# Kernel tuning notes

Measured on AMD Instinct MI355X. Metric: run time of the kernel, lower is better.

Reference implementation:

```python
import jax, jax.numpy as jnp
import numpy as np

N, E, D, H, L = 50000, 800000, 64, 128, 3  # nodes, edges, embed dim, mlp hidden (2*D), layers
HDIM, EDIM, G = 8, 8, 10
EPS_MSG = 1e-7
BN_EPS = 1e-5
LN_EPS = 1e-5


def setup_inputs() -> dict:
    key = jax.random.key(0)
    ks = jax.random.split(key, 12)
    s = lambda f: 1.0 / np.sqrt(f)
    return {
        "x": jax.random.normal(ks[0], (N, HDIM), jnp.float32),
        "edge_index": jax.random.randint(ks[1], (2, E), 0, N, dtype=jnp.int32),
        "edge_attr": jax.random.normal(ks[2], (E, EDIM), jnp.float32),
        "node_W": jax.random.normal(ks[3], (HDIM, D), jnp.float32) * s(HDIM),
        "node_b": jnp.zeros((D,), jnp.float32),
        "edge_W": jax.random.normal(ks[4], (EDIM, D), jnp.float32) * s(EDIM),
        "edge_b": jnp.zeros((D,), jnp.float32),
        "bn_gamma": jnp.ones((L, D), jnp.float32),
        "bn_beta": jnp.zeros((L, D), jnp.float32),
        "t": jnp.ones((L,), jnp.float32),
        "W1": jax.random.normal(ks[5], (L, D, H), jnp.float32) * s(D),
        "b1": jnp.zeros((L, H), jnp.float32),
        "ln_g": jnp.ones((L, H), jnp.float32),
        "ln_b": jnp.zeros((L, H), jnp.float32),
        "W2": jax.random.normal(ks[6], (L, H, D), jnp.float32) * s(H),
        "b2": jnp.zeros((L, D), jnp.float32),
        "num_graphs": G,
    }


def _layer(h, src, dst, e, g, b, t_i, W1i, b1i, lg, lb, W2i, b2i):
    # DeepGCNLayer 'res+': out = x + conv(relu(BN(x)))
    mu = h.mean(0)
    var = h.var(0)  # biased, as torch BN normalization
    hn = jax.nn.relu((h - mu) / jnp.sqrt(var + BN_EPS) * g + b)
    # GENConv message: relu(x_j + edge_attr) + eps
    msg = jax.nn.relu(hn[src] + e) + EPS_MSG  # [E, D]
    # softmax aggregation per destination node, per channel, with temperature t
    logits = msg * t_i
    m = jax.ops.segment_max(logits, dst, num_segments=N)
    m = jnp.where(jnp.isfinite(m), m, 0.0)
    a = jnp.exp(logits - m[dst])
    denom = jax.ops.segment_sum(a, dst, num_segments=N)
    agg = jax.ops.segment_sum(a * msg, dst, num_segments=N)
    agg = agg / jnp.maximum(denom, 1e-16)
    out = agg + hn  # GENConv root residual
    # GENConv MLP [D, 2D, D]: Linear -> LayerNorm -> ReLU -> Linear
    y = out @ W1i + b1i
    mu2 = y.mean(-1, keepdims=True)
    var2 = y.var(-1, keepdims=True)
    y = (y - mu2) / jnp.sqrt(var2 + LN_EPS) * lg + lb
    y = jax.nn.relu(y)
    y = y @ W2i + b2i
    return h + y


def reference(x, edge_index, edge_attr, node_W, node_b, edge_W, edge_b,
              bn_gamma, bn_beta, t, W1, b1, ln_g, ln_b, W2, b2, num_graphs):
    h = x @ node_W + node_b
    e = edge_attr @ edge_W + edge_b
    src, dst = edge_index[0], edge_index[1]
    for i in range(L):
        h = _layer(h, src, dst, e, bn_gamma[i], bn_beta[i], t[i],
                   W1[i], b1[i], ln_g[i], ln_b[i], W2[i], b2[i])
    return h.reshape(num_graphs, -1, D)
```

## Files before the change

kernel.cpp:

```cpp
#include <hip/hip_runtime.h>
#include <hip/hip_bf16.h>
#include <hip/hip_fp16.h>

constexpr int HDIM = 8;
constexpr int EDIM = 8;

typedef _Float16 half8 __attribute__((ext_vector_type(8)));
typedef float f32x4 __attribute__((ext_vector_type(4)));
union H8U { uint4 u; half8 h; };

__device__ __forceinline__ unsigned pack2h(float a, float b) {
  __half2 h = __floats2half2_rn(a, b);
  union { __half2 h2; unsigned u; } u;
  u.h2 = h;
  return u.u;
}

__device__ __forceinline__ __half2 u2h2(unsigned v) {
  union { unsigned u; __half2 h2; } u;
  u.u = v;
  return u.h2;
}

__global__ __launch_bounds__(256) void init_h_stats_kernel(
    const float* __restrict__ x, const float* __restrict__ W, const float* __restrict__ b,
    float* __restrict__ h, float* __restrict__ sums, int* __restrict__ deg, int n) {
  __shared__ float reds[256], redq[256];
  int tid = threadIdx.x, lane = tid & 63;
  int gtid = blockIdx.x * 256 + tid;
  for (int i = gtid; i < n; i += 512 * 256) deg[i] = 0;
  float wc[HDIM];
#pragma unroll
  for (int k = 0; k < HDIM; ++k) wc[k] = W[k * 64 + lane];
  float bc = b[lane];
  float s = 0.f, q = 0.f;
  int total = n * 64;
  for (int gid = gtid; gid < total; gid += 512 * 256) {
    int row = gid >> 6;
    const float* xr = x + (size_t)row * HDIM;
    float acc = bc;
#pragma unroll
    for (int k = 0; k < HDIM; ++k) acc = fmaf(xr[k], wc[k], acc);
    h[gid] = acc;
    s += acc;
    q = fmaf(acc, acc, q);
  }
  reds[tid] = s; redq[tid] = q;
  __syncthreads();
  if (tid < 64) {
    float S = reds[tid] + reds[64 + tid] + reds[128 + tid] + reds[192 + tid];
    float Q = redq[tid] + redq[64 + tid] + redq[128 + tid] + redq[192 + tid];
    int slot = blockIdx.x & 7;
    atomicAdd(&sums[slot * 128 + tid], S);
    atomicAdd(&sums[slot * 128 + 64 + tid], Q);
  }
}

__global__ void deg_kernel(const int* __restrict__ dst, int* __restrict__ deg,
                           int* __restrict__ idxw, int E) {
  int e = blockIdx.x * 256 + threadIdx.x;
  if (e < E) idxw[e] = atomicAdd(&deg[dst[e]], 1);
}

__global__ __launch_bounds__(256) void scan_part_kernel(const int* __restrict__ deg,
                                                        int* __restrict__ partials, int n) {
  __shared__ int sh[256];
  int tid = threadIdx.x, idx = blockIdx.x * 256 + tid;
  int v = (idx < n) ? deg[idx] : 0;
  sh[tid] = v;
  __syncthreads();
  for (int o = 128; o > 0; o >>= 1) {
    if (tid < o) sh[tid] += sh[tid + o];
    __syncthreads();
  }
  if (tid == 0) partials[blockIdx.x] = sh[0];
}

__global__ __launch_bounds__(1024) void scan_top_kernel(int* __restrict__ partials, int nb) {
  __shared__ int sh[1024];
  int tid = threadIdx.x;
  int v = (tid < nb) ? partials[tid] : 0;
  sh[tid] = v;
  __syncthreads();
  for (int o = 1; o < 1024; o <<= 1) {
    int a = (tid >= o) ? sh[tid - o] : 0;
    __syncthreads();
    sh[tid] += a;
    __syncthreads();
  }
  if (tid < nb) partials[tid] = sh[tid] - v;
}

__global__ __launch_bounds__(256) void scan_fill_kernel(
    const int* __restrict__ deg, const int* __restrict__ partials,
    int* __restrict__ rowstart, int n, int total) {
  __shared__ int sh[256];
  int tid = threadIdx.x, idx = blockIdx.x * 256 + tid;
  int v = (idx < n) ? deg[idx] : 0;
  sh[tid] = v;
  __syncthreads();
  for (int o = 1; o < 256; o <<= 1) {
    int a = (tid >= o) ? sh[tid - o] : 0;
    __syncthreads();
    sh[tid] += a;
    __syncthreads();
  }
  if (idx < n) rowstart[idx] = partials[blockIdx.x] + sh[tid] - v;
  if (blockIdx.x == 0 && tid == 0) rowstart[n] = total;
}

__global__ void fill_kernel(const int* __restrict__ src, const int* __restrict__ dst,
                            const int* __restrict__ idxw, const int* __restrict__ rowstart,
                            const float* __restrict__ edge_attr, char* __restrict__ recs, int E) {
  int e = blockIdx.x * 256 + threadIdx.x;
  if (e >= E) return;
  int d = dst[e];
  int slot = rowstart[d] + idxw[e];
  const float4* ap = (const float4*)(edge_attr + (size_t)e * EDIM);
  float4 a = ap[0], c = ap[1];
  uint4 rv;
  rv.x = pack2h(a.x, a.y);
  rv.y = pack2h(a.z, a.w);
  rv.z = pack2h(c.x, c.y);
  rv.w = pack2h(c.z, c.w);
  char* rb = recs + (size_t)slot * 32;
  *(uint4*)rb = rv;
  *(int*)(rb + 16) = src[e];
}

__global__ __launch_bounds__(256) void bn_apply_kernel(
    const float* __restrict__ h, const float* __restrict__ sums,
    const float* __restrict__ bn_g, const float* __restrict__ bn_b,
    unsigned short* __restrict__ hn, int n, float invN) {
  int tid0 = blockIdx.x * 256 + threadIdx.x;
  int lane = tid0 & 63;
  float ssum = 0.f, qsum = 0.f;
#pragma unroll
  for (int k = 0; k < 8; ++k) {
    ssum += sums[k * 128 + lane];
    qsum += sums[k * 128 + 64 + lane];
  }
  float mu = ssum * invN;
  float var = qsum * invN - mu * mu;
  float a = rsqrtf(var + 1e-5f) * bn_g[lane];
  float c = bn_b[lane] - mu * a;
  int total = n * 64;
  for (int gid = tid0; gid < total; gid += 512 * 256) {
    float v = fmaxf(fmaf(h[gid], a, c), 0.f);
    hn[gid] = __half_as_ushort(__float2half(v));
  }
}

__global__ __launch_bounds__(256) void aggregate_kernel(
    const unsigned short* __restrict__ hn, const int* __restrict__ rowstart,
    const char* __restrict__ recs, const float* __restrict__ edge_W,
    const float* __restrict__ edge_b, const float* __restrict__ t,
    float* __restrict__ out, int n) {
  int lane = threadIdx.x & 63;
  int node = blockIdx.x * 4 + (threadIdx.x >> 6);
  if (node >= n) return;
  __half2 wc2[4];
#pragma unroll
  for (int k = 0; k < 4; ++k)
    wc2[k] = __floats2half2_rn(edge_W[(2 * k) * 64 + lane], edge_W[(2 * k + 1) * 64 + lane]);
  float eb = edge_b[lane];
  float tt = t[0];
  int s0 = __builtin_amdgcn_readfirstlane(rowstart[node]);
  int s1 = __builtin_amdgcn_readfirstlane(rowstart[node + 1]);
  float hd = __half2float(__ushort_as_half(hn[(size_t)node * 64 + lane]));
  float den = 0.f, num = 0.f;
#define EDGE_STEP(HU, RV)                                                      \
  {                                                                            \
    __half2 acc = __hmul2(u2h2(RV.w), wc2[3]);                                 \
    acc = __hfma2(u2h2(RV.z), wc2[2], acc);                                    \
    acc = __hfma2(u2h2(RV.y), wc2[1], acc);                                    \
    acc = __hfma2(u2h2(RV.x), wc2[0], acc);                                    \
    float ev = __low2float(acc) + __high2float(acc) + eb;                      \
    float hnv = __half2float(__ushort_as_half(HU));                            \
    float msg = fmaxf(hnv + ev, 0.f) + 1e-7f;                                  \
    float p = __expf(msg * tt);                                                \
    den += p;                                                                  \
    num = fmaf(p, msg, num);                                                   \
  }
  int j = s0;
  for (; j + 8 <= s1; j += 8) {
    const char* rb = recs + (size_t)j * 32;
    uint4 r0 = *(const uint4*)(rb);
    uint4 r1 = *(const uint4*)(rb + 32);
    uint4 r2 = *(const uint4*)(rb + 64);
    uint4 r3 = *(const uint4*)(rb + 96);
    uint4 r4 = *(const uint4*)(rb + 128);
    uint4 r5 = *(const uint4*)(rb + 160);
    uint4 r6 = *(const uint4*)(rb + 192);
    uint4 r7 = *(const uint4*)(rb + 224);
    int i0 = *(const int*)(rb + 16);
    int i1 = *(const int*)(rb + 48);
    int i2 = *(const int*)(rb + 80);
    int i3 = *(const int*)(rb + 112);
    int i4 = *(const int*)(rb + 144);
    int i5 = *(const int*)(rb + 176);
    int i6 = *(const int*)(rb + 208);
    int i7 = *(const int*)(rb + 240);
    unsigned short u0 = hn[(size_t)i0 * 64 + lane];
    unsigned short u1 = hn[(size_t)i1 * 64 + lane];
    unsigned short u2 = hn[(size_t)i2 * 64 + lane];
    unsigned short u3 = hn[(size_t)i3 * 64 + lane];
    unsigned short u4 = hn[(size_t)i4 * 64 + lane];
    unsigned short u5 = hn[(size_t)i5 * 64 + lane];
    unsigned short u6 = hn[(size_t)i6 * 64 + lane];
    unsigned short u7 = hn[(size_t)i7 * 64 + lane];
    EDGE_STEP(u0, r0)
    EDGE_STEP(u1, r1)
    EDGE_STEP(u2, r2)
    EDGE_STEP(u3, r3)
    EDGE_STEP(u4, r4)
    EDGE_STEP(u5, r5)
    EDGE_STEP(u6, r6)
    EDGE_STEP(u7, r7)
  }
  for (; j + 4 <= s1; j += 4) {
    const char* rb = recs + (size_t)j * 32;
    uint4 r0 = *(const uint4*)(rb);
    uint4 r1 = *(const uint4*)(rb + 32);
    uint4 r2 = *(const uint4*)(rb + 64);
    uint4 r3 = *(const uint4*)(rb + 96);
    int i0 = *(const int*)(rb + 16);
    int i1 = *(const int*)(rb + 48);
    int i2 = *(const int*)(rb + 80);
    int i3 = *(const int*)(rb + 112);
    unsigned short u0 = hn[(size_t)i0 * 64 + lane];
    unsigned short u1 = hn[(size_t)i1 * 64 + lane];
    unsigned short u2 = hn[(size_t)i2 * 64 + lane];
    unsigned short u3 = hn[(size_t)i3 * 64 + lane];
    EDGE_STEP(u0, r0)
    EDGE_STEP(u1, r1)
    EDGE_STEP(u2, r2)
    EDGE_STEP(u3, r3)
  }
  for (; j < s1; ++j) {
    const char* rb = recs + (size_t)j * 32;
    uint4 r0 = *(const uint4*)(rb);
    int i0 = *(const int*)(rb + 16);
    unsigned short u0 = hn[(size_t)i0 * 64 + lane];
    EDGE_STEP(u0, r0)
  }
#undef EDGE_STEP
  out[(size_t)node * 64 + lane] = num / fmaxf(den, 1e-16f) + hd;
}

__global__ __launch_bounds__(256) void mlp_mfma_kernel(
    const float* __restrict__ outv, const float* __restrict__ h_in,
    const float* __restrict__ W1, const float* __restrict__ b1,
    const float* __restrict__ lng, const float* __restrict__ lnb,
    const float* __restrict__ W2, const float* __restrict__ b2,
    float* __restrict__ h_out, float* __restrict__ nextsums, int n) {
  __shared__ uint4 lds[2560];
  const int tid = threadIdx.x;
  const int wv = tid >> 6, l = tid & 63;
  const int n0 = blockIdx.x * 64;
  uint4* XA = lds;
  uint4* WB = lds + 512;
  uint4* ZF = lds + 1536;
#pragma unroll
  for (int i = 0; i < 2; ++i) {
    int c = tid + i * 256;
    int node = c >> 3, k8 = c & 7;
    int nd = n0 + node;
    half8 hv;
    if (nd < n) {
      const float* xp = outv + (size_t)nd * 64 + k8 * 8;
#pragma unroll
      for (int j = 0; j < 8; ++j) hv[j] = (_Float16)xp[j];
    } else {
#pragma unroll
      for (int j = 0; j < 8; ++j) hv[j] = (_Float16)0.f;
    }
    H8U u; u.h = hv;
    int mt = node >> 4, kt = k8 >> 2;
    int lanep = ((k8 & 3) << 4) | (node & 15);
    XA[(mt * 2 + kt) * 64 + lanep] = u.u;
  }
#pragma unroll
  for (int i = 0; i < 4; ++i) {
    int c = tid + i * 256;
    int fid = c >> 6, lp = c & 63;
    int nt = fid >> 1, kt = fid & 1;
    int ncol = (nt << 4) | (lp & 15);
    int k0 = kt * 32 + (lp >> 4) * 8;
    half8 hv;
#pragma unroll
    for (int j = 0; j < 8; ++j) hv[j] = (_Float16)W1[(size_t)(k0 + j) * 128 + ncol];
    H8U u; u.h = hv;
    WB[fid * 64 + lp] = u.u;
  }
  __syncthreads();
  f32x4 cfr[8];
#pragma unroll
  for (int nt = 0; nt < 8; ++nt) cfr[nt] = (f32x4){0.f, 0.f, 0.f, 0.f};
  {
    H8U a0, a1;
    a0.u = XA[(wv * 2 + 0) * 64 + l];
    a1.u = XA[(wv * 2 + 1) * 64 + l];
#pragma unroll
    for (int nt = 0; nt < 8; ++nt) {
      H8U b0, b1u;
      b0.u = WB[(nt * 2 + 0) * 64 + l];
      b1u.u = WB[(nt * 2 + 1) * 64 + l];
      cfr[nt] = __builtin_amdgcn_mfma_f32_16x16x32_f16(a0.h, b0.h, cfr[nt], 0, 0, 0);
      cfr[nt] = __builtin_amdgcn_mfma_f32_16x16x32_f16(a1.h, b1u.h, cfr[nt], 0, 0, 0);
    }
  }
  int col = l & 15;
  float s4[4] = {0.f, 0.f, 0.f, 0.f}, q4[4] = {0.f, 0.f, 0.f, 0.f};
#pragma unroll
  for (int nt = 0; nt < 8; ++nt) {
    float bb = b1[nt * 16 + col];
#pragma unroll
    for (int r = 0; r < 4; ++r) {
      float v = cfr[nt][r] + bb;
      cfr[nt][r] = v;
      s4[r] += v;
      q4[r] = fmaf(v, v, q4[r]);
    }
  }
#pragma unroll
  for (int off = 1; off < 16; off <<= 1) {
#pragma unroll
    for (int r = 0; r < 4; ++r) {
      s4[r] += __shfl_xor(s4[r], off, 64);
      q4[r] += __shfl_xor(q4[r], off, 64);
    }
  }
  float mu4[4], rs4[4];
#pragma unroll
  for (int r = 0; r < 4; ++r) {
    float mu = s4[r] * (1.f / 128.f);
    float var = q4[r] * (1.f / 128.f) - mu * mu;
    mu4[r] = mu;
    rs4[r] = rsqrtf(var + 1e-5f);
  }
  {
    unsigned short* ZB = (unsigned short*)ZF;
#pragma unroll
    for (int nt = 0; nt < 8; ++nt) {
      int ch = nt * 16 + col;
      int kt2 = ch >> 5, kl = ch & 31;
      float g = lng[ch], bb = lnb[ch];
#pragma unroll
      for (int r = 0; r < 4; ++r) {
        int row = (l >> 4) * 4 + r;
        float zv = fmaxf((cfr[nt][r] - mu4[r]) * rs4[r] * g + bb, 0.f);
        int lanep = ((kl >> 3) << 4) | row;
        ZB[((wv * 4 + kt2) * 64 + lanep) * 8 + (kl & 7)] = __half_as_ushort(__float2half(zv));
      }
    }
  }
  __syncthreads();
#pragma unroll
  for (int i = 0; i < 4; ++i) {
    int c = tid + i * 256;
    int fid = c >> 6, lp = c & 63;
    int nt2 = fid >> 2, kt2 = fid & 3;
    int ncol = (nt2 << 4) | (lp & 15);
    int k0 = kt2 * 32 + (lp >> 4) * 8;
    half8 hv;
#pragma unroll
    for (int j = 0; j < 8; ++j) hv[j] = (_Float16)W2[(size_t)(k0 + j) * 64 + ncol];
    H8U u; u.h = hv;
    WB[fid * 64 + lp] = u.u;
  }
  __syncthreads();
  f32x4 dfr[4];
#pragma unroll
  for (int nt2 = 0; nt2 < 4; ++nt2) dfr[nt2] = (f32x4){0.f, 0.f, 0.f, 0.f};
  {
    H8U za[4];
#pragma unroll
    for (int kt2 = 0; kt2 < 4; ++kt2) za[kt2].u = ZF[(wv * 4 + kt2) * 64 + l];
#pragma unroll
    for (int nt2 = 0; nt2 < 4; ++nt2) {
#pragma unroll
      for (int kt2 = 0; kt2 < 4; ++kt2) {
        H8U bu;
        bu.u = WB[(nt2 * 4 + kt2) * 64 + l];
        dfr[nt2] = __builtin_amdgcn_mfma_f32_16x16x32_f16(za[kt2].h, bu.h, dfr[nt2], 0, 0, 0);
      }
    }
  }
  float ssum[4] = {0.f, 0.f, 0.f, 0.f}, qsum[4] = {0.f, 0.f, 0.f, 0.f};
#pragma unroll
  for (int nt2 = 0; nt2 < 4; ++nt2) {
    int ch2 = nt2 * 16 + col;
    float bb = b2[ch2];
#pragma unroll
    for (int r = 0; r < 4; ++r) {
      int nd = n0 + wv * 16 + (l >> 4) * 4 + r;
      if (nd < n) {
        float v = h_in[(size_t)nd * 64 + ch2] + dfr[nt2][r] + bb;
        h_out[(size_t)nd * 64 + ch2] = v;
        ssum[nt2] += v;
        qsum[nt2] = fmaf(v, v, qsum[nt2]);
      }
    }
  }
  if (nextsums != nullptr) {
#pragma unroll
    for (int nt2 = 0; nt2 < 4; ++nt2) {
      ssum[nt2] += __shfl_xor(ssum[nt2], 16, 64);
      ssum[nt2] += __shfl_xor(ssum[nt2], 32, 64);
      qsum[nt2] += __shfl_xor(qsum[nt2], 16, 64);
      qsum[nt2] += __shfl_xor(qsum[nt2], 32, 64);
    }
    float* SS = (float*)(ZF + wv * 256);
    if (l < 16) {
#pragma unroll
      for (int nt2 = 0; nt2 < 4; ++nt2) {
        SS[nt2 * 16 + l] = ssum[nt2];
        SS[64 + nt2 * 16 + l] = qsum[nt2];
      }
    }
    __syncthreads();
    if (tid < 64) {
      float S = 0.f, Q = 0.f;
#pragma unroll
      for (int w = 0; w < 4; ++w) {
        const float* P = (const float*)(ZF + w * 256);
        S += P[tid];
        Q += P[64 + tid];
      }
      int slot = blockIdx.x & 7;
      atomicAdd(&nextsums[slot * 128 + tid], S);
      atomicAdd(&nextsums[slot * 128 + 64 + tid], Q);
    }
  }
}

extern "C" void kernel_launch(void* const* d_in, const int* in_sizes, int n_in,
                              void* d_out, int out_size, void* d_ws, size_t ws_size,
                              hipStream_t stream) {
  const float* x = (const float*)d_in[0];
  const int* edge_index = (const int*)d_in[1];
  const float* edge_attr = (const float*)d_in[2];
  const float* node_W = (const float*)d_in[3];
  const float* node_b = (const float*)d_in[4];
  const float* edge_W = (const float*)d_in[5];
  const float* edge_b = (const float*)d_in[6];
  const float* bn_g = (const float*)d_in[7];
  const float* bn_b = (const float*)d_in[8];
  const float* t = (const float*)d_in[9];
  const float* W1 = (const float*)d_in[10];
  const float* b1 = (const float*)d_in[11];
  const float* ln_g = (const float*)d_in[12];
  const float* ln_b = (const float*)d_in[13];
  const float* W2 = (const float*)d_in[14];
  const float* b2 = (const float*)d_in[15];

  int N = in_sizes[0] / HDIM;
  int E = in_sizes[1] / 2;
  const int* srcp = edge_index;
  const int* dstp = edge_index + E;

  char* ws = (char*)d_ws;
  size_t off = 0;
  auto alloc = [&](size_t bytes) {
    char* p = ws + off;
    off = (off + bytes + 255) & ~(size_t)255;
    return p;
  };
  int* deg = (int*)alloc((size_t)N * 4);
  int* rowstart = (int*)alloc(((size_t)N + 1) * 4);
  int* idxw = (int*)alloc((size_t)E * 4);
  int* partials = (int*)alloc(1024 * 4);
  float* bnsums = (float*)alloc(3 * 1024 * 4);
  char* recs = (char*)alloc((size_t)E * 32);
  float* h = (float*)alloc((size_t)N * 64 * 4);
  float* outv = (float*)alloc((size_t)N * 64 * 4);
  unsigned short* hn = (unsigned short*)alloc((size_t)N * 64 * 2);
  (void)ws_size; (void)n_in; (void)out_size;

  int nb = (N + 255) / 256;
  hipMemsetAsync(bnsums, 0, 3 * 1024 * 4, stream);
  init_h_stats_kernel<<<512, 256, 0, stream>>>(x, node_W, node_b, h, bnsums, deg, N);
  deg_kernel<<<(E + 255) / 256, 256, 0, stream>>>(dstp, deg, idxw, E);
  scan_part_kernel<<<nb, 256, 0, stream>>>(deg, partials, N);
  scan_top_kernel<<<1, 1024, 0, stream>>>(partials, nb);
  scan_fill_kernel<<<nb, 256, 0, stream>>>(deg, partials, rowstart, N, E);
  fill_kernel<<<(E + 255) / 256, 256, 0, stream>>>(srcp, dstp, idxw, rowstart, edge_attr, recs, E);

  float invN = 1.0f / (float)N;
  int mlp_blocks = (N + 63) / 64;
  for (int l = 0; l < 3; ++l) {
    bn_apply_kernel<<<512, 256, 0, stream>>>(h, bnsums + l * 1024, bn_g + l * 64,
                                             bn_b + l * 64, hn, N, invN);
    aggregate_kernel<<<(N + 3) / 4, 256, 0, stream>>>(hn, rowstart, recs, edge_W, edge_b,
                                                      t + l, outv, N);
    float* hout = (l == 2) ? (float*)d_out : h;
    float* nxt = (l == 2) ? nullptr : (bnsums + (l + 1) * 1024);
    mlp_mfma_kernel<<<mlp_blocks, 256, 0, stream>>>(outv, h, W1 + (size_t)l * 8192, b1 + l * 128,
                                                    ln_g + l * 128, ln_b + l * 128,
                                                    W2 + (size_t)l * 8192, b2 + l * 64, hout, nxt, N);
  }
}
```

Baseline: 266.5 us.

## Fuse batchnorm apply into aggregation and store node state in fp16

Removes the separate BN-apply kernel and instead applies the BN affine transform plus ReLU on the fly to each gathered neighbour row inside the aggregation kernel. Node state h and the aggregated output are now stored as fp16 instead of fp32, halving gather, MLP-input and residual traffic. The MLP kernel now reads fp16 inputs directly and writes fp16 h, except in the final layer, which writes fp32 output. The costs are an extra FMA and max per edge, and a loss of precision because the residual stream is carried in half precision across layers.

Result: faster. 254.8 us (-4.4%).

```diff
diff --git a/kernel.cpp b/kernel.cpp
--- a/kernel.cpp
+++ b/kernel.cpp
@@ -24,7 +24,7 @@
 
 __global__ __launch_bounds__(256) void init_h_stats_kernel(
     const float* __restrict__ x, const float* __restrict__ W, const float* __restrict__ b,
-    float* __restrict__ h, float* __restrict__ sums, int* __restrict__ deg, int n) {
+    unsigned short* __restrict__ h, float* __restrict__ sums, int* __restrict__ deg, int n) {
   __shared__ float reds[256], redq[256];
   int tid = threadIdx.x, lane = tid & 63;
   int gtid = blockIdx.x * 256 + tid;
@@ -41,7 +41,7 @@
     float acc = bc;
 #pragma unroll
     for (int k = 0; k < HDIM; ++k) acc = fmaf(xr[k], wc[k], acc);
-    h[gid] = acc;
+    h[gid] = __half_as_ushort(__float2half(acc));
     s += acc;
     q = fmaf(acc, acc, q);
   }
@@ -128,12 +128,15 @@
   *(int*)(rb + 16) = src[e];
 }
 
-__global__ __launch_bounds__(256) void bn_apply_kernel(
-    const float* __restrict__ h, const float* __restrict__ sums,
+__global__ __launch_bounds__(256) void aggregate_kernel(
+    const unsigned short* __restrict__ h, const float* __restrict__ sums,
     const float* __restrict__ bn_g, const float* __restrict__ bn_b,
-    unsigned short* __restrict__ hn, int n, float invN) {
-  int tid0 = blockIdx.x * 256 + threadIdx.x;
-  int lane = tid0 & 63;
+    const int* __restrict__ rowstart, const char* __restrict__ recs,
+    const float* __restrict__ edge_W, const float* __restrict__ edge_b,
+    const float* __restrict__ t, unsigned short* __restrict__ out, int n, float invN) {
+  int lane = threadIdx.x & 63;
+  int node = blockIdx.x * 4 + (threadIdx.x >> 6);
+  if (node >= n) return;
   float ssum = 0.f, qsum = 0.f;
 #pragma unroll
   for (int k = 0; k < 8; ++k) {
@@ -142,23 +145,8 @@
   }
   float mu = ssum * invN;
   float var = qsum * invN - mu * mu;
-  float a = rsqrtf(var + 1e-5f) * bn_g[lane];
-  float c = bn_b[lane] - mu * a;
-  int total = n * 64;
-  for (int gid = tid0; gid < total; gid += 512 * 256) {
-    float v = fmaxf(fmaf(h[gid], a, c), 0.f);
-    hn[gid] = __half_as_ushort(__float2half(v));
-  }
-}
-
-__global__ __launch_bounds__(256) void aggregate_kernel(
-    const unsigned short* __restrict__ hn, const int* __restrict__ rowstart,
-    const char* __restrict__ recs, const float* __restrict__ edge_W,
-    const float* __restrict__ edge_b, const float* __restrict__ t,
-    float* __restrict__ out, int n) {
-  int lane = threadIdx.x & 63;
-  int node = blockIdx.x * 4 + (threadIdx.x >> 6);
-  if (node >= n) return;
+  float aa = rsqrtf(var + 1e-5f) * bn_g[lane];
+  float cc = bn_b[lane] - mu * aa;
   __half2 wc2[4];
 #pragma unroll
   for (int k = 0; k < 4; ++k)
@@ -167,7 +155,7 @@
   float tt = t[0];
   int s0 = __builtin_amdgcn_readfirstlane(rowstart[node]);
   int s1 = __builtin_amdgcn_readfirstlane(rowstart[node + 1]);
-  float hd = __half2float(__ushort_as_half(hn[(size_t)node * 64 + lane]));
+  float hd = fmaxf(fmaf(__half2float(__ushort_as_half(h[(size_t)node * 64 + lane])), aa, cc), 0.f);
   float den = 0.f, num = 0.f;
 #define EDGE_STEP(HU, RV)                                                      \
   {                                                                            \
@@ -176,7 +164,7 @@
     acc = __hfma2(u2h2(RV.y), wc2[1], acc);                                    \
     acc = __hfma2(u2h2(RV.x), wc2[0], acc);                                    \
     float ev = __low2float(acc) + __high2float(acc) + eb;                      \
-    float hnv = __half2float(__ushort_as_half(HU));                            \
+    float hnv = fmaxf(fmaf(__half2float(__ushort_as_half(HU)), aa, cc), 0.f);  \
     float msg = fmaxf(hnv + ev, 0.f) + 1e-7f;                                  \
     float p = __expf(msg * tt);                                                \
     den += p;                                                                  \
@@ -201,14 +189,14 @@
     int i5 = *(const int*)(rb + 176);
     int i6 = *(const int*)(rb + 208);
     int i7 = *(const int*)(rb + 240);
-    unsigned short u0 = hn[(size_t)i0 * 64 + lane];
-    unsigned short u1 = hn[(size_t)i1 * 64 + lane];
-    unsigned short u2 = hn[(size_t)i2 * 64 + lane];
-    unsigned short u3 = hn[(size_t)i3 * 64 + lane];
-    unsigned short u4 = hn[(size_t)i4 * 64 + lane];
-    unsigned short u5 = hn[(size_t)i5 * 64 + lane];
-    unsigned short u6 = hn[(size_t)i6 * 64 + lane];
-    unsigned short u7 = hn[(size_t)i7 * 64 + lane];
+    unsigned short u0 = h[(size_t)i0 * 64 + lane];
+    unsigned short u1 = h[(size_t)i1 * 64 + lane];
+    unsigned short u2 = h[(size_t)i2 * 64 + lane];
+    unsigned short u3 = h[(size_t)i3 * 64 + lane];
+    unsigned short u4 = h[(size_t)i4 * 64 + lane];
+    unsigned short u5 = h[(size_t)i5 * 64 + lane];
+    unsigned short u6 = h[(size_t)i6 * 64 + lane];
+    unsigned short u7 = h[(size_t)i7 * 64 + lane];
     EDGE_STEP(u0, r0)
     EDGE_STEP(u1, r1)
     EDGE_STEP(u2, r2)
@@ -228,10 +216,10 @@
     int i1 = *(const int*)(rb + 48);
     int i2 = *(const int*)(rb + 80);
     int i3 = *(const int*)(rb + 112);
-    unsigned short u0 = hn[(size_t)i0 * 64 + lane];
-    unsigned short u1 = hn[(size_t)i1 * 64 + lane];
-    unsigned short u2 = hn[(size_t)i2 * 64 + lane];
-    unsigned short u3 = hn[(size_t)i3 * 64 + lane];
+    unsigned short u0 = h[(size_t)i0 * 64 + lane];
+    unsigned short u1 = h[(size_t)i1 * 64 + lane];
+    unsigned short u2 = h[(size_t)i2 * 64 + lane];
+    unsigned short u3 = h[(size_t)i3 * 64 + lane];
     EDGE_STEP(u0, r0)
     EDGE_STEP(u1, r1)
     EDGE_STEP(u2, r2)
@@ -241,19 +229,21 @@
     const char* rb = recs + (size_t)j * 32;
     uint4 r0 = *(const uint4*)(rb);
     int i0 = *(const int*)(rb + 16);
-    unsigned short u0 = hn[(size_t)i0 * 64 + lane];
+    unsigned short u0 = h[(size_t)i0 * 64 + lane];
     EDGE_STEP(u0, r0)
   }
 #undef EDGE_STEP
-  out[(size_t)node * 64 + lane] = num / fmaxf(den, 1e-16f) + hd;
+  float res = num / fmaxf(den, 1e-16f) + hd;
+  out[(size_t)node * 64 + lane] = __half_as_ushort(__float2half(res));
 }
 
 __global__ __launch_bounds__(256) void mlp_mfma_kernel(
-    const float* __restrict__ outv, const float* __restrict__ h_in,
+    const unsigned short* __restrict__ outv, const unsigned short* __restrict__ h_in,
     const float* __restrict__ W1, const float* __restrict__ b1,
     const float* __restrict__ lng, const float* __restrict__ lnb,
     const float* __restrict__ W2, const float* __restrict__ b2,
-    float* __restrict__ h_out, float* __restrict__ nextsums, int n) {
+    unsigned short* __restrict__ hout16, float* __restrict__ hout32,
+    float* __restrict__ nextsums, int n) {
   __shared__ uint4 lds[2560];
   const int tid = threadIdx.x;
   const int wv = tid >> 6, l = tid & 63;
@@ -266,19 +256,15 @@
     int c = tid + i * 256;
     int node = c >> 3, k8 = c & 7;
     int nd = n0 + node;
-    half8 hv;
+    uint4 u;
     if (nd < n) {
-      const float* xp = outv + (size_t)nd * 64 + k8 * 8;
-#pragma unroll
-      for (int j = 0; j < 8; ++j) hv[j] = (_Float16)xp[j];
+      u = *(const uint4*)(outv + (size_t)nd * 64 + k8 * 8);
     } else {
-#pragma unroll
-      for (int j = 0; j < 8; ++j) hv[j] = (_Float16)0.f;
-    }
-    H8U u; u.h = hv;
+      u = make_uint4(0, 0, 0, 0);
+    }
     int mt = node >> 4, kt = k8 >> 2;
     int lanep = ((k8 & 3) << 4) | (node & 15);
-    XA[(mt * 2 + kt) * 64 + lanep] = u.u;
+    XA[(mt * 2 + kt) * 64 + lanep] = u;
   }
 #pragma unroll
   for (int i = 0; i < 4; ++i) {
@@ -396,8 +382,13 @@
     for (int r = 0; r < 4; ++r) {
       int nd = n0 + wv * 16 + (l >> 4) * 4 + r;
       if (nd < n) {
-        float v = h_in[(size_t)nd * 64 + ch2] + dfr[nt2][r] + bb;
-        h_out[(size_t)nd * 64 + ch2] = v;
+        float hv = __half2float(__ushort_as_half(h_in[(size_t)nd * 64 + ch2]));
+        float v = hv + dfr[nt2][r] + bb;
+        if (hout32 != nullptr) {
+          hout32[(size_t)nd * 64 + ch2] = v;
+        } else {
+          hout16[(size_t)nd * 64 + ch2] = __half_as_ushort(__float2half(v));
+        }
         ssum[nt2] += v;
         qsum[nt2] = fmaf(v, v, qsum[nt2]);
       }
@@ -473,9 +464,8 @@
   int* partials = (int*)alloc(1024 * 4);
   float* bnsums = (float*)alloc(3 * 1024 * 4);
   char* recs = (char*)alloc((size_t)E * 32);
-  float* h = (float*)alloc((size_t)N * 64 * 4);
-  float* outv = (float*)alloc((size_t)N * 64 * 4);
-  unsigned short* hn = (unsigned short*)alloc((size_t)N * 64 * 2);
+  unsigned short* h = (unsigned short*)alloc((size_t)N * 64 * 2);
+  unsigned short* outv = (unsigned short*)alloc((size_t)N * 64 * 2);
   (void)ws_size; (void)n_in; (void)out_size;
 
   int nb = (N + 255) / 256;
@@ -490,14 +480,15 @@
   float invN = 1.0f / (float)N;
   int mlp_blocks = (N + 63) / 64;
   for (int l = 0; l < 3; ++l) {
-    bn_apply_kernel<<<512, 256, 0, stream>>>(h, bnsums + l * 1024, bn_g + l * 64,
-                                             bn_b + l * 64, hn, N, invN);
-    aggregate_kernel<<<(N + 3) / 4, 256, 0, stream>>>(hn, rowstart, recs, edge_W, edge_b,
-                                                      t + l, outv, N);
-    float* hout = (l == 2) ? (float*)d_out : h;
+    aggregate_kernel<<<(N + 3) / 4, 256, 0, stream>>>(
+        h, bnsums + l * 1024, bn_g + l * 64, bn_b + l * 64, rowstart, recs,
+        edge_W, edge_b, t + l, outv, N, invN);
+    unsigned short* h16 = (l == 2) ? nullptr : h;
+    float* h32 = (l == 2) ? (float*)d_out : nullptr;
     float* nxt = (l == 2) ? nullptr : (bnsums + (l + 1) * 1024);
     mlp_mfma_kernel<<<mlp_blocks, 256, 0, stream>>>(outv, h, W1 + (size_t)l * 8192, b1 + l * 128,
                                                     ln_g + l * 128, ln_b + l * 128,
-                                                    W2 + (size_t)l * 8192, b2 + l * 64, hout, nxt, N);
-  }
-}
+                                                    W2 + (size_t)l * 8192, b2 + l * 64,
+                                                    h16, h32, nxt, N);
+  }
+}
```
